# Kernel tuning notes

Measured on AMD Instinct MI355X. Metric: run time of the kernel, lower is better.

Reference implementation:

```python
import jax, jax.numpy as jnp
import numpy as np

NEG_SLOPE = 0.2


def _gat_layer(x, W, a_src, a_dst, b, src, dst, n_nodes, heads, dim):
    # x: [N, F_in]; W: [F_in, heads*dim]
    h = (x @ W).reshape(n_nodes, heads, dim)            # [N,H,D]
    e_src = (h * a_src).sum(-1)                          # [N,H]
    e_dst = (h * a_dst).sum(-1)                          # [N,H]
    e = jax.nn.leaky_relu(e_src[src] + e_dst[dst], NEG_SLOPE)  # [E,H]
    # edge softmax over incoming edges of each target node
    m = jax.ops.segment_max(e, dst, num_segments=n_nodes)      # [N,H]
    ex = jnp.exp(e - m[dst])
    denom = jax.ops.segment_sum(ex, dst, num_segments=n_nodes)  # [N,H]
    alpha = ex / denom[dst]                              # [E,H]
    out = jax.ops.segment_sum(h[src] * alpha[:, :, None], dst,
                              num_segments=n_nodes)      # [N,H,D]
    return out.reshape(n_nodes, heads * dim) + b


def setup_inputs() -> dict:
    key = jax.random.key(0)
    ks = jax.random.split(key, 10)
    N, E, F_in = 100000, 1600000, 300
    x = jax.random.normal(ks[0], (N, F_in), dtype=jnp.float32)
    edge_index = jax.random.randint(ks[1], (2, E), 0, N, dtype=jnp.int64)
    s = 0.1
    return {
        'x': x,
        'edge_index': edge_index,
        'W1': jax.random.normal(ks[2], (F_in, 64), jnp.float32) * s,
        'att_src1': jax.random.normal(ks[3], (8, 8), jnp.float32) * s,
        'att_dst1': jax.random.normal(ks[4], (8, 8), jnp.float32) * s,
        'b1': jax.random.normal(ks[5], (64,), jnp.float32) * s,
        'W2': jax.random.normal(ks[6], (64, 64), jnp.float32) * s,
        'att_src2': jax.random.normal(ks[7], (1, 64), jnp.float32) * s,
        'att_dst2': jax.random.normal(ks[8], (1, 64), jnp.float32) * s,
        'b2': jax.random.normal(ks[9], (64,), jnp.float32) * s,
    }


def reference(x, edge_index, W1, att_src1, att_dst1, b1, W2, att_src2, att_dst2, b2):
    N = x.shape[0]
    # add self-loops (PyG GATConv default)
    loop = jnp.arange(N, dtype=edge_index.dtype)
    src = jnp.concatenate([edge_index[0], loop])
    dst = jnp.concatenate([edge_index[1], loop])
    # dropout p=0.6 is identity in eval mode
    h = _gat_layer(x, W1, att_src1, att_dst1, b1, src, dst, N, 8, 8)    # [N,64]
    h = jax.nn.elu(h)
    h = _gat_layer(h, W2, att_src2, att_dst2, b2, src, dst, N, 1, 64)   # [N,64]
    return jax.nn.log_softmax(h, axis=1)
```

## Files before the change

### kernel.cpp

```cpp
#include <hip/hip_runtime.h>
#include <math.h>

using short8  = __attribute__((ext_vector_type(8))) short;
using ushort8 = __attribute__((ext_vector_type(8))) unsigned short;
using f32x4   = __attribute__((ext_vector_type(4))) float;

#define NBLKS 512
#define BPAD  800
#define EB 4
#define HSTR 80

__device__ __forceinline__ unsigned short f2bf(float f) {
    unsigned u = __float_as_uint(f);
    unsigned r = u + 0x7FFF + ((u >> 16) & 1);
    return (unsigned short)(r >> 16);
}
__device__ __forceinline__ float bf2f(unsigned short v) {
    return __uint_as_float((unsigned)v << 16);
}
__device__ __forceinline__ unsigned cvt2(float lo, float hi) {
    unsigned r;
    asm("v_cvt_pk_bf16_f32 %0, %1, %2" : "=v"(r) : "v"(lo), "v"(hi));
    return r;
}


__global__ void detect64_kernel(const int* __restrict__ ei, int E, int* __restrict__ flag) {
    __shared__ int any;
    if (threadIdx.x == 0) any = 0;
    __syncthreads();
    for (int i = threadIdx.x; i < 1024; i += 256) {
        if (ei[2 * i + 1] != 0) { any = 1; break; }
    }
    __syncthreads();
    if (threadIdx.x == 0) *flag = (any ? 0 : 1);
}


__global__ __launch_bounds__(256) void binA_kernel(
    const int* __restrict__ ei, int E, int N, const int* __restrict__ flag,
    int nbuck, int* __restrict__ hist, int chunk) {
    __shared__ int lh[BPAD];
    for (int i = threadIdx.x; i < nbuck; i += 256) lh[i] = 0;
    __syncthreads();
    int is64 = *flag;
    int Etot = E + N;
    int beg = blockIdx.x * chunk, end = min(Etot, beg + chunk);
    for (int i = beg + threadIdx.x; i < end; i += 256) {
        int d = (i < E) ? (is64 ? ei[2 * (E + i)] : ei[E + i]) : (i - E);
        atomicAdd(&lh[d >> 7], 1);
    }
    __syncthreads();
    for (int i = threadIdx.x; i < nbuck; i += 256) hist[blockIdx.x * BPAD + i] = lh[i];
}

__global__ void scanBlocks_kernel(int* __restrict__ hist, int nbuck, int* __restrict__ bucketTotal) {
    int bin = blockIdx.x * 256 + threadIdx.x;
    if (bin >= nbuck) return;
    int run = 0;
    for (int b = 0; b < NBLKS; b++) {
        int v = hist[b * BPAD + bin];
        hist[b * BPAD + bin] = run;
        run += v;
    }
    bucketTotal[bin] = run;
}

__global__ void scanBucket_kernel(const int* __restrict__ bucketTotal, int nbuck,
                                  int* __restrict__ bucketBase) {
    __shared__ int s[1024];
    int t = threadIdx.x;
    int v = (t < nbuck) ? bucketTotal[t] : 0;
    s[t] = v;
    __syncthreads();
    for (int off = 1; off < 1024; off <<= 1) {
        int x = (t >= off) ? s[t - off] : 0;
        __syncthreads();
        s[t] += x;
        __syncthreads();
    }
    if (t < nbuck) bucketBase[t] = s[t] - v;
    if (t == nbuck - 1) bucketBase[nbuck] = s[t];
}

__global__ __launch_bounds__(256) void binB_kernel(
    const int* __restrict__ ei, int E, int N, const int* __restrict__ flag,
    int nbuck, const int* __restrict__ hist, const int* __restrict__ bucketBase,
    int* __restrict__ tmp, int chunk) {
    __shared__ int cur[BPAD];
    for (int i = threadIdx.x; i < nbuck; i += 256)
        cur[i] = bucketBase[i] + hist[blockIdx.x * BPAD + i];
    __syncthreads();
    int is64 = *flag;
    int Etot = E + N;
    int beg = blockIdx.x * chunk, end = min(Etot, beg + chunk);
    for (int i = beg + threadIdx.x; i < end; i += 256) {
        int s, d;
        if (i < E) {
            if (is64) { s = ei[2 * i]; d = ei[2 * (E + i)]; }
            else      { s = ei[i];     d = ei[E + i]; }
        } else { s = i - E; d = i - E; }
        int pos = atomicAdd(&cur[d >> 7], 1);
        tmp[pos] = ((d & 127) << 17) | s;
    }
}

__global__ __launch_bounds__(256) void binC_kernel(
    const int* __restrict__ tmp, const int* __restrict__ bucketBase, int nbuck,
    int N, int Etot, int* __restrict__ rowptr, int* __restrict__ col) {
    __shared__ int lh[128];
    __shared__ int cur[128];
    int g = blockIdx.x;
    int t = threadIdx.x;
    int beg = bucketBase[g], end = bucketBase[g + 1];
    if (t < 128) lh[t] = 0;
    __syncthreads();
    for (int i = beg + t; i < end; i += 256) atomicAdd(&lh[tmp[i] >> 17], 1);
    __syncthreads();
    int c = (t < 128) ? lh[t] : 0;
    for (int off = 1; off < 128; off <<= 1) {
        int x = 0;
        if (t < 128 && t >= off) x = lh[t - off];
        __syncthreads();
        if (t < 128) lh[t] += x;
        __syncthreads();
    }
    if (t < 128) {
        int excl = lh[t] - c;
        cur[t] = beg + excl;
        int node = g * 128 + t;
        if (node < N) rowptr[node] = beg + excl;
    }
    if (g == 0 && t == 0) rowptr[N] = Etot;
    if (g == 0 && t < 64) col[Etot + t] = 0;
    __syncthreads();
    for (int i = beg + t; i < end; i += 256) {
        int v = tmp[i];
        int pos = atomicAdd(&cur[v >> 17], 1);
        col[pos] = v & 0x1FFFF;
    }
}


__global__ __launch_bounds__(256) void gemm1_mfma_kernel(
    const float* __restrict__ x, const float* __restrict__ W,
    const float* __restrict__ asrc, const float* __restrict__ adst,
    unsigned short* __restrict__ hbf, float* __restrict__ ed, int N) {
    __shared__ __align__(16) unsigned short A_lds[64 * 40];
    __shared__ __align__(16) unsigned short B_lds[64 * 40];
    const int tx = threadIdx.x;
    const int wv = tx >> 6;
    const int lane = tx & 63;
    const int l15 = lane & 15;
    const int quad = lane >> 4;
    const int rowBase = blockIdx.x * 64;

    f32x4 acc[4];
#pragma unroll
    for (int ct = 0; ct < 4; ct++) acc[ct] = (f32x4){0.f, 0.f, 0.f, 0.f};

    const int kq = tx & 7;
    const int r0 = tx >> 3;
    const int colB = tx & 63;
    const int kkb = (tx >> 6) * 8;

    for (int k0 = 0; k0 < 320; k0 += 32) {
        bool kvalid = (k0 + kq * 4 + 4 <= 300);
#pragma unroll
        for (int p = 0; p < 2; p++) {
            int row = p * 32 + r0;
            int grow = rowBase + row;
            float4 v = make_float4(0.f, 0.f, 0.f, 0.f);
            if (kvalid && grow < N) v = *(const float4*)&x[(size_t)grow * 300 + k0 + kq * 4];
            *(uint2*)&A_lds[row * 40 + kq * 4] = make_uint2(cvt2(v.x, v.y), cvt2(v.z, v.w));
        }
        {
            float v0, v1, v2, v3, v4, v5, v6, v7;
            v0 = (k0 + kkb + 0 < 300) ? W[(size_t)(k0 + kkb + 0) * 64 + colB] : 0.f;
            v1 = (k0 + kkb + 1 < 300) ? W[(size_t)(k0 + kkb + 1) * 64 + colB] : 0.f;
            v2 = (k0 + kkb + 2 < 300) ? W[(size_t)(k0 + kkb + 2) * 64 + colB] : 0.f;
            v3 = (k0 + kkb + 3 < 300) ? W[(size_t)(k0 + kkb + 3) * 64 + colB] : 0.f;
            v4 = (k0 + kkb + 4 < 300) ? W[(size_t)(k0 + kkb + 4) * 64 + colB] : 0.f;
            v5 = (k0 + kkb + 5 < 300) ? W[(size_t)(k0 + kkb + 5) * 64 + colB] : 0.f;
            v6 = (k0 + kkb + 6 < 300) ? W[(size_t)(k0 + kkb + 6) * 64 + colB] : 0.f;
            v7 = (k0 + kkb + 7 < 300) ? W[(size_t)(k0 + kkb + 7) * 64 + colB] : 0.f;
            *(uint2*)&B_lds[colB * 40 + kkb]     = make_uint2(cvt2(v0, v1), cvt2(v2, v3));
            *(uint2*)&B_lds[colB * 40 + kkb + 4] = make_uint2(cvt2(v4, v5), cvt2(v6, v7));
        }
        __syncthreads();
        short8 af, bfr[4];
        af = *(const short8*)&A_lds[(wv * 16 + l15) * 40 + quad * 8];
#pragma unroll
        for (int ct = 0; ct < 4; ct++)
            bfr[ct] = *(const short8*)&B_lds[(ct * 16 + l15) * 40 + quad * 8];
#pragma unroll
        for (int ct = 0; ct < 4; ct++)
            acc[ct] = __builtin_amdgcn_mfma_f32_16x16x32_bf16(af, bfr[ct], acc[ct], 0, 0, 0);
        __syncthreads();
    }

    float as_v[4], ad_v[4];
#pragma unroll
    for (int ct = 0; ct < 4; ct++) {
        as_v[ct] = asrc[ct * 16 + l15];
        ad_v[ct] = adst[ct * 16 + l15];
    }
#pragma unroll
    for (int reg = 0; reg < 4; reg++) {
        int row = rowBase + wv * 16 + quad * 4 + reg;
        bool ok = (row < N);
#pragma unroll
        for (int ct = 0; ct < 4; ct++) {
            float v = acc[ct][reg];
            if (ok) hbf[(size_t)row * HSTR + ct * 16 + l15] = f2bf(v);
            float ps = v * as_v[ct];
            float pd = v * ad_v[ct];
            ps += __shfl_xor(ps, 1); ps += __shfl_xor(ps, 2); ps += __shfl_xor(ps, 4);
            pd += __shfl_xor(pd, 1); pd += __shfl_xor(pd, 2); pd += __shfl_xor(pd, 4);
            if ((lane & 7) == 0 && ok) {
                int head = 2 * ct + ((lane >> 3) & 1);
                *(float*)((char*)hbf + (size_t)row * (HSTR * 2) + 128 + 4 * head) = ps;
                ed[row * 8 + head] = pd;
            }
        }
    }
}


__global__ __launch_bounds__(256) void gemm2_mfma_kernel(
    const unsigned short* __restrict__ xin, const float* __restrict__ W,
    const float* __restrict__ asrc, const float* __restrict__ adst,
    unsigned short* __restrict__ hbf, float* __restrict__ ed, int N) {
    __shared__ __align__(16) unsigned short A_lds[128 * 72];
    __shared__ __align__(16) unsigned short B_lds[64 * 72];
    const int tx = threadIdx.x;
    const int wv = tx >> 6;
    const int lane = tx & 63;
    const int l15 = lane & 15;
    const int quad = lane >> 4;
    const int rowBase = blockIdx.x * 128;

    f32x4 acc[2][4];
#pragma unroll
    for (int rt = 0; rt < 2; rt++)
#pragma unroll
        for (int ct = 0; ct < 4; ct++) acc[rt][ct] = (f32x4){0.f, 0.f, 0.f, 0.f};

    {
        int colB = tx & 63;
        int kk = (tx >> 6) * 16;
#pragma unroll
        for (int j = 0; j < 16; j++)
            B_lds[colB * 72 + kk + j] = f2bf(W[(size_t)(kk + j) * 64 + colB]);
    }
    {
        int kq = tx & 7, r0 = tx >> 3;
        const ushort8 z = (ushort8){0, 0, 0, 0, 0, 0, 0, 0};
#pragma unroll
        for (int p = 0; p < 4; p++) {
            int row = p * 32 + r0;
            int grow = rowBase + row;
            ushort8 v = z;
            if (grow < N) v = *(const ushort8*)&xin[(size_t)grow * 64 + kq * 8];
            *(ushort8*)&A_lds[row * 72 + kq * 8] = v;
        }
    }
    __syncthreads();
#pragma unroll
    for (int c = 0; c < 2; c++) {
        short8 af[2], bfr[4];
#pragma unroll
        for (int rt = 0; rt < 2; rt++)
            af[rt] = *(const short8*)&A_lds[(wv * 32 + rt * 16 + l15) * 72 + quad * 8 + c * 32];
#pragma unroll
        for (int ct = 0; ct < 4; ct++)
            bfr[ct] = *(const short8*)&B_lds[(ct * 16 + l15) * 72 + quad * 8 + c * 32];
#pragma unroll
        for (int rt = 0; rt < 2; rt++)
#pragma unroll
            for (int ct = 0; ct < 4; ct++)
                acc[rt][ct] = __builtin_amdgcn_mfma_f32_16x16x32_bf16(af[rt], bfr[ct], acc[rt][ct], 0, 0, 0);
    }

    float as_v[4], ad_v[4];
#pragma unroll
    for (int ct = 0; ct < 4; ct++) {
        as_v[ct] = asrc[ct * 16 + l15];
        ad_v[ct] = adst[ct * 16 + l15];
    }
#pragma unroll
    for (int rt = 0; rt < 2; rt++) {
#pragma unroll
        for (int reg = 0; reg < 4; reg++) {
            int row = rowBase + wv * 32 + rt * 16 + quad * 4 + reg;
            bool ok = (row < N);
            float ps = 0.f, pd = 0.f;
#pragma unroll
            for (int ct = 0; ct < 4; ct++) {
                float v = acc[rt][ct][reg];
                if (ok) hbf[(size_t)row * HSTR + ct * 16 + l15] = f2bf(v);
                ps = fmaf(v, as_v[ct], ps);
                pd = fmaf(v, ad_v[ct], pd);
            }
            ps += __shfl_xor(ps, 1); ps += __shfl_xor(ps, 2);
            ps += __shfl_xor(ps, 4); ps += __shfl_xor(ps, 8);
            pd += __shfl_xor(pd, 1); pd += __shfl_xor(pd, 2);
            pd += __shfl_xor(pd, 4); pd += __shfl_xor(pd, 8);
            if (l15 == 0 && ok) {
                *(float*)((char*)hbf + (size_t)row * (HSTR * 2) + 128) = ps;
                ed[row] = pd;
            }
        }
    }
}


__global__ __launch_bounds__(256) void agg1f_kernel(
    const int* __restrict__ rowptr, const int* __restrict__ col,
    const unsigned short* __restrict__ hbf, const float* __restrict__ ed,
    const float* __restrict__ b, unsigned int* __restrict__ outbf, int N) {
    int node = blockIdx.x * 4 + (threadIdx.x >> 6);
    int lane = threadIdx.x & 63;
    if (node >= N) return;
    int half = lane >> 5, fl = lane & 31;
    int f0 = fl * 2, hh = fl >> 2;
    int beg = rowptr[node], end = rowptr[node + 1];
    float edv = ed[node * 8 + hh];
    const char* hb = (const char*)hbf;
    float acc0 = 0.f, acc1 = 0.f, lsum = 0.f;
    for (int i0 = beg; i0 < end; i0 += 64) {
        int idx = i0 + lane;
        int cv = col[idx < end ? idx : beg];
        int lim = min(64, end - i0);
        for (int s = 0; s < lim; s += 8) {
            int ss[EB], vld[EB];
            float ev[EB];
            unsigned hp[EB];
#pragma unroll
            for (int j = 0; j < EB; j++) {
                int sl = s + 2 * j + half;
                ss[j] = __shfl(cv, sl);
                vld[j] = (i0 + sl < end);
            }
#pragma unroll
            for (int j = 0; j < EB; j++)
                ev[j] = *(const float*)(hb + (size_t)ss[j] * (HSTR * 2) + 128 + 4 * hh);
#pragma unroll
            for (int j = 0; j < EB; j++)
                hp[j] = *(const unsigned*)(hb + (size_t)ss[j] * (HSTR * 2) + 4 * fl);
#pragma unroll
            for (int j = 0; j < EB; j++) {
                float e = ev[j] + edv;
                e = (e > 0.f) ? e : 0.2f * e;
                float wj = __expf(fminf(e, 30.f));
                wj = vld[j] ? wj : 0.f;
                lsum += wj;
                float lo = __uint_as_float(hp[j] << 16);
                float hi = __uint_as_float(hp[j] & 0xFFFF0000u);
                acc0 = fmaf(wj, lo, acc0);
                acc1 = fmaf(wj, hi, acc1);
            }
        }
    }
    acc0 += __shfl_xor(acc0, 32);
    acc1 += __shfl_xor(acc1, 32);
    lsum += __shfl_xor(lsum, 32);
    float rinv = 1.f / lsum;
    float o0 = acc0 * rinv + b[f0];
    float o1 = acc1 * rinv + b[f0 + 1];
    o0 = (o0 > 0.f) ? o0 : expm1f(o0);
    o1 = (o1 > 0.f) ? o1 : expm1f(o1);
    if (half == 0) {
        unsigned pk = (unsigned)f2bf(o0) | ((unsigned)f2bf(o1) << 16);
        outbf[((size_t)node * 64 + f0) >> 1] = pk;
    }
}

__global__ __launch_bounds__(256) void agg2f_kernel(
    const int* __restrict__ rowptr, const int* __restrict__ col,
    const unsigned short* __restrict__ hbf, const float* __restrict__ ed,
    const float* __restrict__ b, float* __restrict__ out, int N) {
    int node = blockIdx.x * 4 + (threadIdx.x >> 6);
    int lane = threadIdx.x & 63;
    if (node >= N) return;
    int half = lane >> 5, fl = lane & 31;
    int f0 = fl * 2;
    int beg = rowptr[node], end = rowptr[node + 1];
    float edv = ed[node];
    const char* hb = (const char*)hbf;
    float acc0 = 0.f, acc1 = 0.f, lsum = 0.f;
    for (int i0 = beg; i0 < end; i0 += 64) {
        int idx = i0 + lane;
        int cv = col[idx < end ? idx : beg];
        int lim = min(64, end - i0);
        for (int s = 0; s < lim; s += 8) {
            int ss[EB], vld[EB];
            float ev[EB];
            unsigned hp[EB];
#pragma unroll
            for (int j = 0; j < EB; j++) {
                int sl = s + 2 * j + half;
                ss[j] = __shfl(cv, sl);
                vld[j] = (i0 + sl < end);
            }
#pragma unroll
            for (int j = 0; j < EB; j++)
                ev[j] = *(const float*)(hb + (size_t)ss[j] * (HSTR * 2) + 128);
#pragma unroll
            for (int j = 0; j < EB; j++)
                hp[j] = *(const unsigned*)(hb + (size_t)ss[j] * (HSTR * 2) + 4 * fl);
#pragma unroll
            for (int j = 0; j < EB; j++) {
                float e = ev[j] + edv;
                e = (e > 0.f) ? e : 0.2f * e;
                float wj = __expf(fminf(e, 30.f));
                wj = vld[j] ? wj : 0.f;
                lsum += wj;
                float lo = __uint_as_float(hp[j] << 16);
                float hi = __uint_as_float(hp[j] & 0xFFFF0000u);
                acc0 = fmaf(wj, lo, acc0);
                acc1 = fmaf(wj, hi, acc1);
            }
        }
    }
    acc0 += __shfl_xor(acc0, 32);
    acc1 += __shfl_xor(acc1, 32);
    lsum += __shfl_xor(lsum, 32);
    float rinv = 1.f / lsum;
    float o0 = acc0 * rinv + b[f0];
    float o1 = acc1 * rinv + b[f0 + 1];
    float M = fmaxf(o0, o1);
    M = fmaxf(M, __shfl_xor(M, 1));  M = fmaxf(M, __shfl_xor(M, 2));
    M = fmaxf(M, __shfl_xor(M, 4));  M = fmaxf(M, __shfl_xor(M, 8));
    M = fmaxf(M, __shfl_xor(M, 16));
    float se = __expf(o0 - M) + __expf(o1 - M);
    se += __shfl_xor(se, 1);  se += __shfl_xor(se, 2);
    se += __shfl_xor(se, 4);  se += __shfl_xor(se, 8);
    se += __shfl_xor(se, 16);
    float ls = logf(se);
    if (half == 0) {
        float2 r = make_float2(o0 - M - ls, o1 - M - ls);
        *(float2*)&out[(size_t)node * 64 + f0] = r;
    }
}


extern "C" void kernel_launch(void* const* d_in, const int* in_sizes, int n_in,
                              void* d_out, int out_size, void* d_ws, size_t ws_size,
                              hipStream_t stream) {
    const float* x   = (const float*)d_in[0];
    const int*   ei  = (const int*)d_in[1];
    const float* W1  = (const float*)d_in[2];
    const float* as1 = (const float*)d_in[3];
    const float* ad1 = (const float*)d_in[4];
    const float* b1  = (const float*)d_in[5];
    const float* W2  = (const float*)d_in[6];
    const float* as2 = (const float*)d_in[7];
    const float* ad2 = (const float*)d_in[8];
    const float* b2  = (const float*)d_in[9];
    const int N = in_sizes[0] / 300;
    const int E = in_sizes[1] / 2;
    const int Etot = E + N;
    const int nbuck = (N + 127) >> 7;
    (void)n_in; (void)out_size; (void)ws_size;

    char* w = (char*)d_ws;
    auto alloc = [&](size_t bytes) -> char* {
        char* p = w;
        w += (bytes + 255) & ~(size_t)255;
        return p;
    };
    int*   flag        = (int*)alloc(256);
    int*   hist        = (int*)alloc((size_t)NBLKS * BPAD * 4);
    int*   bucketTotal = (int*)alloc((size_t)(BPAD + 1) * 4);
    int*   bucketBase  = (int*)alloc((size_t)(BPAD + 1) * 4);
    int*   tmp         = (int*)alloc((size_t)(Etot + 64) * 4);
    int*   rowptr      = (int*)alloc((size_t)(N + 1) * 4);
    int*   col         = (int*)alloc((size_t)(Etot + 64) * 4);
    unsigned short* h1x = (unsigned short*)alloc((size_t)N * HSTR * 2);
    unsigned short* h1p = (unsigned short*)alloc((size_t)N * 64 * 2);
    float* ed1         = (float*)alloc((size_t)N * 8 * 4);
    float* ed2         = (float*)alloc((size_t)N * 4);
    unsigned short* h2x = h1x;

    detect64_kernel<<<1, 256, 0, stream>>>(ei, E, flag);

    int chunk = (Etot + NBLKS - 1) / NBLKS;
    binA_kernel<<<NBLKS, 256, 0, stream>>>(ei, E, N, flag, nbuck, hist, chunk);
    scanBlocks_kernel<<<(nbuck + 255) / 256, 256, 0, stream>>>(hist, nbuck, bucketTotal);
    scanBucket_kernel<<<1, 1024, 0, stream>>>(bucketTotal, nbuck, bucketBase);
    binB_kernel<<<NBLKS, 256, 0, stream>>>(ei, E, N, flag, nbuck, hist, bucketBase, tmp, chunk);
    binC_kernel<<<nbuck, 256, 0, stream>>>(tmp, bucketBase, nbuck, N, Etot, rowptr, col);

    gemm1_mfma_kernel<<<(N + 63) / 64, 256, 0, stream>>>(x, W1, as1, ad1, h1x, ed1, N);
    agg1f_kernel<<<(N + 3) / 4, 256, 0, stream>>>(rowptr, col, h1x, ed1, b1,
                                                  (unsigned int*)h1p, N);
    gemm2_mfma_kernel<<<(N + 127) / 128, 256, 0, stream>>>(h1p, W2, as2, ad2, h2x, ed2, N);
    agg2f_kernel<<<(N + 3) / 4, 256, 0, stream>>>(rowptr, col, h2x, ed2, b2, (float*)d_out, N);
}
```

Baseline: 433.3 us.

## Software-pipeline neighbor gathers in aggregation kernels and inline int64 detection

The aggregation kernels now prefetch the next group of neighbor feature and score loads while computing on the current group, using a double-buffered register pipeline to hide gather latency. The separate detect64 kernel launch is removed, and each binning block re-derives the int64 flag itself from the first 1024 edge entries. This saves one launch and a dependency, but every binning block now does extra redundant reads. The prefetch also raises register pressure, which may reduce occupancy.

```diff
diff --git a/kernel.cpp b/kernel.cpp
--- a/kernel.cpp
+++ b/kernel.cpp
@@ -25,25 +25,18 @@
 }
 
 
-__global__ void detect64_kernel(const int* __restrict__ ei, int E, int* __restrict__ flag) {
-    __shared__ int any;
-    if (threadIdx.x == 0) any = 0;
-    __syncthreads();
-    for (int i = threadIdx.x; i < 1024; i += 256) {
-        if (ei[2 * i + 1] != 0) { any = 1; break; }
-    }
-    __syncthreads();
-    if (threadIdx.x == 0) *flag = (any ? 0 : 1);
-}
-
-
 __global__ __launch_bounds__(256) void binA_kernel(
-    const int* __restrict__ ei, int E, int N, const int* __restrict__ flag,
+    const int* __restrict__ ei, int E, int N,
     int nbuck, int* __restrict__ hist, int chunk) {
     __shared__ int lh[BPAD];
+    __shared__ int sflag;
+    if (threadIdx.x == 0) sflag = 0;
     for (int i = threadIdx.x; i < nbuck; i += 256) lh[i] = 0;
     __syncthreads();
-    int is64 = *flag;
+    for (int i = threadIdx.x; i < 1024; i += 256)
+        if (ei[2 * i + 1] != 0) sflag = 1;
+    __syncthreads();
+    int is64 = (sflag == 0);
     int Etot = E + N;
     int beg = blockIdx.x * chunk, end = min(Etot, beg + chunk);
     for (int i = beg + threadIdx.x; i < end; i += 256) {
@@ -84,14 +77,19 @@
 }
 
 __global__ __launch_bounds__(256) void binB_kernel(
-    const int* __restrict__ ei, int E, int N, const int* __restrict__ flag,
+    const int* __restrict__ ei, int E, int N,
     int nbuck, const int* __restrict__ hist, const int* __restrict__ bucketBase,
     int* __restrict__ tmp, int chunk) {
     __shared__ int cur[BPAD];
+    __shared__ int sflag;
+    if (threadIdx.x == 0) sflag = 0;
     for (int i = threadIdx.x; i < nbuck; i += 256)
         cur[i] = bucketBase[i] + hist[blockIdx.x * BPAD + i];
     __syncthreads();
-    int is64 = *flag;
+    for (int i = threadIdx.x; i < 1024; i += 256)
+        if (ei[2 * i + 1] != 0) sflag = 1;
+    __syncthreads();
+    int is64 = (sflag == 0);
     int Etot = E + N;
     int beg = blockIdx.x * chunk, end = min(Etot, beg + chunk);
     for (int i = beg + threadIdx.x; i < end; i += 256) {
@@ -332,34 +330,40 @@
         int idx = i0 + lane;
         int cv = col[idx < end ? idx : beg];
         int lim = min(64, end - i0);
+        float evA[EB] = {0.f, 0.f, 0.f, 0.f};
+        unsigned hpA[EB] = {0, 0, 0, 0};
+#pragma unroll
+        for (int j = 0; j < EB; j++) {
+            int ssj = __shfl(cv, 2 * j + half);
+            evA[j] = *(const float*)(hb + (size_t)ssj * (HSTR * 2) + 128 + 4 * hh);
+            hpA[j] = *(const unsigned*)(hb + (size_t)ssj * (HSTR * 2) + 4 * fl);
+        }
         for (int s = 0; s < lim; s += 8) {
-            int ss[EB], vld[EB];
-            float ev[EB];
-            unsigned hp[EB];
+            float evB[EB] = {0.f, 0.f, 0.f, 0.f};
+            unsigned hpB[EB] = {0, 0, 0, 0};
+            int sn = s + 8;
+            if (sn < lim) {
+#pragma unroll
+                for (int j = 0; j < EB; j++) {
+                    int ssj = __shfl(cv, sn + 2 * j + half);
+                    evB[j] = *(const float*)(hb + (size_t)ssj * (HSTR * 2) + 128 + 4 * hh);
+                    hpB[j] = *(const unsigned*)(hb + (size_t)ssj * (HSTR * 2) + 4 * fl);
+                }
+            }
 #pragma unroll
             for (int j = 0; j < EB; j++) {
-                int sl = s + 2 * j + half;
-                ss[j] = __shfl(cv, sl);
-                vld[j] = (i0 + sl < end);
-            }
-#pragma unroll
-            for (int j = 0; j < EB; j++)
-                ev[j] = *(const float*)(hb + (size_t)ss[j] * (HSTR * 2) + 128 + 4 * hh);
-#pragma unroll
-            for (int j = 0; j < EB; j++)
-                hp[j] = *(const unsigned*)(hb + (size_t)ss[j] * (HSTR * 2) + 4 * fl);
-#pragma unroll
-            for (int j = 0; j < EB; j++) {
-                float e = ev[j] + edv;
+                float e = evA[j] + edv;
                 e = (e > 0.f) ? e : 0.2f * e;
                 float wj = __expf(fminf(e, 30.f));
-                wj = vld[j] ? wj : 0.f;
+                wj = (i0 + s + 2 * j + half < end) ? wj : 0.f;
                 lsum += wj;
-                float lo = __uint_as_float(hp[j] << 16);
-                float hi = __uint_as_float(hp[j] & 0xFFFF0000u);
+                float lo = __uint_as_float(hpA[j] << 16);
+                float hi = __uint_as_float(hpA[j] & 0xFFFF0000u);
                 acc0 = fmaf(wj, lo, acc0);
                 acc1 = fmaf(wj, hi, acc1);
             }
+#pragma unroll
+            for (int j = 0; j < EB; j++) { evA[j] = evB[j]; hpA[j] = hpB[j]; }
         }
     }
     acc0 += __shfl_xor(acc0, 32);
@@ -393,34 +397,40 @@
         int idx = i0 + lane;
         int cv = col[idx < end ? idx : beg];
         int lim = min(64, end - i0);
+        float evA[EB] = {0.f, 0.f, 0.f, 0.f};
+        unsigned hpA[EB] = {0, 0, 0, 0};
+#pragma unroll
+        for (int j = 0; j < EB; j++) {
+            int ssj = __shfl(cv, 2 * j + half);
+            evA[j] = *(const float*)(hb + (size_t)ssj * (HSTR * 2) + 128);
+            hpA[j] = *(const unsigned*)(hb + (size_t)ssj * (HSTR * 2) + 4 * fl);
+        }
         for (int s = 0; s < lim; s += 8) {
-            int ss[EB], vld[EB];
-            float ev[EB];
-            unsigned hp[EB];
+            float evB[EB] = {0.f, 0.f, 0.f, 0.f};
+            unsigned hpB[EB] = {0, 0, 0, 0};
+            int sn = s + 8;
+            if (sn < lim) {
+#pragma unroll
+                for (int j = 0; j < EB; j++) {
+                    int ssj = __shfl(cv, sn + 2 * j + half);
+                    evB[j] = *(const float*)(hb + (size_t)ssj * (HSTR * 2) + 128);
+                    hpB[j] = *(const unsigned*)(hb + (size_t)ssj * (HSTR * 2) + 4 * fl);
+                }
+            }
 #pragma unroll
             for (int j = 0; j < EB; j++) {
-                int sl = s + 2 * j + half;
-                ss[j] = __shfl(cv, sl);
-                vld[j] = (i0 + sl < end);
-            }
-#pragma unroll
-            for (int j = 0; j < EB; j++)
-                ev[j] = *(const float*)(hb + (size_t)ss[j] * (HSTR * 2) + 128);
-#pragma unroll
-            for (int j = 0; j < EB; j++)
-                hp[j] = *(const unsigned*)(hb + (size_t)ss[j] * (HSTR * 2) + 4 * fl);
-#pragma unroll
-            for (int j = 0; j < EB; j++) {
-                float e = ev[j] + edv;
+                float e = evA[j] + edv;
                 e = (e > 0.f) ? e : 0.2f * e;
                 float wj = __expf(fminf(e, 30.f));
-                wj = vld[j] ? wj : 0.f;
+                wj = (i0 + s + 2 * j + half < end) ? wj : 0.f;
                 lsum += wj;
-                float lo = __uint_as_float(hp[j] << 16);
-                float hi = __uint_as_float(hp[j] & 0xFFFF0000u);
+                float lo = __uint_as_float(hpA[j] << 16);
+                float hi = __uint_as_float(hpA[j] & 0xFFFF0000u);
                 acc0 = fmaf(wj, lo, acc0);
                 acc1 = fmaf(wj, hi, acc1);
             }
+#pragma unroll
+            for (int j = 0; j < EB; j++) { evA[j] = evB[j]; hpA[j] = hpB[j]; }
         }
     }
     acc0 += __shfl_xor(acc0, 32);
@@ -470,7 +480,6 @@
         w += (bytes + 255) & ~(size_t)255;
         return p;
     };
-    int*   flag        = (int*)alloc(256);
     int*   hist        = (int*)alloc((size_t)NBLKS * BPAD * 4);
     int*   bucketTotal = (int*)alloc((size_t)(BPAD + 1) * 4);
     int*   bucketBase  = (int*)alloc((size_t)(BPAD + 1) * 4);
@@ -483,13 +492,11 @@
     float* ed2         = (float*)alloc((size_t)N * 4);
     unsigned short* h2x = h1x;
 
-    detect64_kernel<<<1, 256, 0, stream>>>(ei, E, flag);
-
     int chunk = (Etot + NBLKS - 1) / NBLKS;
-    binA_kernel<<<NBLKS, 256, 0, stream>>>(ei, E, N, flag, nbuck, hist, chunk);
+    binA_kernel<<<NBLKS, 256, 0, stream>>>(ei, E, N, nbuck, hist, chunk);
     scanBlocks_kernel<<<(nbuck + 255) / 256, 256, 0, stream>>>(hist, nbuck, bucketTotal);
     scanBucket_kernel<<<1, 1024, 0, stream>>>(bucketTotal, nbuck, bucketBase);
-    binB_kernel<<<NBLKS, 256, 0, stream>>>(ei, E, N, flag, nbuck, hist, bucketBase, tmp, chunk);
+    binB_kernel<<<NBLKS, 256, 0, stream>>>(ei, E, N, nbuck, hist, bucketBase, tmp, chunk);
     binC_kernel<<<nbuck, 256, 0, stream>>>(tmp, bucketBase, nbuck, N, Etot, rowptr, col);
 
     gemm1_mfma_kernel<<<(N + 63) / 64, 256, 0, stream>>>(x, W1, as1, ad1, h1x, ed1, N);
```

Measured after the change: 434.2 us. About the same (+0.2%).
